# Kernel tuning notes

Hardware: AMD Instinct MI355X
Metric: run time of the kernel (lower is better)

Reference implementation:

```python
import jax, jax.numpy as jnp
import numpy as np

EPS = 1e-5  # BatchNorm eps (torch default)


def setup_inputs() -> dict:
    B, C, H, W = 8, 256, 128, 128
    Cr = C // 4
    key = jax.random.key(0)
    ks = jax.random.split(key, 12)
    s = lambda *sh: 1.0 / np.sqrt(np.prod(sh[1:]) if len(sh) > 1 else sh[0])
    return {
        "x": jax.random.normal(ks[0], (B, C, H, W), jnp.float32),
        "text_feat": jax.random.normal(ks[1], (B, C), jnp.float32),
        # spatial_proj: Conv2d(C,C,1) + BatchNorm2d(C) (eval-mode running stats)
        "proj_w": jax.random.normal(ks[2], (C, C), jnp.float32) * s(C, C),
        "proj_b": jax.random.normal(ks[3], (C,), jnp.float32) * 0.02,
        "bn_gamma": jnp.ones((C,), jnp.float32),
        "bn_beta": jnp.zeros((C,), jnp.float32),
        "bn_mean": jnp.zeros((C,), jnp.float32),
        "bn_var": jnp.ones((C,), jnp.float32),
        # channel_attention: Conv2d(C,C/4,1) -> ReLU -> Conv2d(C/4,C,1) -> Sigmoid
        "ca_w1": jax.random.normal(ks[4], (Cr, C), jnp.float32) * s(Cr, C),
        "ca_b1": jax.random.normal(ks[5], (Cr,), jnp.float32) * 0.02,
        "ca_w2": jax.random.normal(ks[6], (C, Cr), jnp.float32) * s(C, Cr),
        "ca_b2": jax.random.normal(ks[7], (C,), jnp.float32) * 0.02,
        # spatial_attention: Conv2d(2,1,7,padding=3) -> Sigmoid
        "sa_w": jax.random.normal(ks[8], (1, 2, 7, 7), jnp.float32) * s(1, 2 * 49),
        "sa_b": jax.random.normal(ks[9], (1,), jnp.float32) * 0.02,
    }


def _forward(x, text_feat, proj_w, proj_b, bn_gamma, bn_beta, bn_mean, bn_var,
             ca_w1, ca_b1, ca_w2, ca_b2, sa_w, sa_b):
    B, C, H, W = x.shape
    # spatial_proj on the spatially-constant broadcast of text_feat: 1x1 conv + BN
    # + ReLU are pointwise, so compute once per (B,C) vector and broadcast.
    t = jnp.einsum('oc,bc->bo', proj_w, text_feat) + proj_b          # (B,C)
    t = (t - bn_mean) * (bn_gamma / jnp.sqrt(bn_var + EPS)) + bn_beta
    t = jax.nn.relu(t)                                               # (B,C)
    # channel attention: global-avg-pool of a constant map is the value itself
    h = jax.nn.relu(jnp.einsum('rc,bc->br', ca_w1, t) + ca_b1)       # (B,C/4)
    channel_weight = jax.nn.sigmoid(jnp.einsum('cr,br->bc', ca_w2, h) + ca_b2)  # (B,C)
    # spatial attention: channel mean/max are per-batch constants, but the 7x7
    # zero-padded conv has edge effects, so run the real conv on broadcast maps.
    avg_feat = jnp.mean(t, axis=1)                                   # (B,)
    max_feat = jnp.max(t, axis=1)                                    # (B,)
    am = jnp.broadcast_to(jnp.stack([avg_feat, max_feat], axis=1)[:, :, None, None],
                          (B, 2, H, W))                              # (B,2,H,W)
    sw = jax.lax.conv_general_dilated(
        am, sa_w, window_strides=(1, 1), padding=((3, 3), (3, 3)),
        dimension_numbers=('NCHW', 'OIHW', 'NCHW')) + sa_b[None, :, None, None]
    spatial_weight = jax.nn.sigmoid(sw)                              # (B,1,H,W)
    return x * channel_weight[:, :, None, None] * spatial_weight


def reference(x, text_feat, proj_w, proj_b, bn_gamma, bn_beta, bn_mean, bn_var,
              ca_w1, ca_b1, ca_w2, ca_b2, sa_w, sa_b):
    return _forward(x, text_feat, proj_w, proj_b, bn_gamma, bn_beta, bn_mean,
                    bn_var, ca_w1, ca_b1, ca_w2, ca_b2, sa_w, sa_b)
```

## Files before the change

### kernel.cpp

```cpp
#include <hip/hip_runtime.h>
#include <math.h>

#define B 8
#define C 256
#define CR 64
#define H 128
#define W 128
#define HW (H*W)
#define NELEM (B*C*HW)
#define N4 (NELEM/4)
#define PER_BATCH4 (C*HW/4)
#define FUSE_BLOCKS_X 1024
#define FUSE_ITERS 4
#define FUSE_STRIDE (FUSE_BLOCKS_X*256)

typedef float floatx4 __attribute__((ext_vector_type(4)));

__device__ __forceinline__ float sigmoidf_(float z) {
    return 1.0f / (1.0f + expf(-z));
}

__global__ __launch_bounds__(256)
void setup_kernel(const float* __restrict__ tf,
                  const float* __restrict__ pw,
                  const float* __restrict__ pb,
                  const float* __restrict__ g,
                  const float* __restrict__ be,
                  const float* __restrict__ mu,
                  const float* __restrict__ var,
                  const float* __restrict__ w1,
                  const float* __restrict__ b1,
                  const float* __restrict__ w2,
                  const float* __restrict__ b2,
                  const float* __restrict__ saw,
                  const float* __restrict__ sab,
                  float* __restrict__ cw,
                  float* __restrict__ tbl)
{
    const int b   = blockIdx.x;
    const int tid = threadIdx.x;

    __shared__ float tf_sh[C];
    __shared__ float t_sh[C];
    __shared__ float h_sh[CR];
    __shared__ float red[8];
    __shared__ float s_stats[2];
    __shared__ float saw_sh[98];

    tf_sh[tid] = tf[b * C + tid];
    if (tid < 98) saw_sh[tid] = saw[tid];
    __syncthreads();

    float acc = 0.0f;
    {
        const float4* pwr = reinterpret_cast<const float4*>(pw + tid * C);
        #pragma unroll 16
        for (int k4 = 0; k4 < C / 4; ++k4) {
            const float4 wv = pwr[k4];
            const float* tfk = &tf_sh[k4 * 4];
            acc += wv.x * tfk[0] + wv.y * tfk[1] + wv.z * tfk[2] + wv.w * tfk[3];
        }
    }
    float t;
    {
        const float scale = g[tid] * rsqrtf(var[tid] + 1e-5f);
        t = (acc + pb[tid] - mu[tid]) * scale + be[tid];
        t = fmaxf(t, 0.0f);
        t_sh[tid] = t;
    }

    {
        float s = t, m = t;
        #pragma unroll
        for (int off = 32; off > 0; off >>= 1) {
            s += __shfl_down(s, off);
            m  = fmaxf(m, __shfl_down(m, off));
        }
        const int wv_ = tid >> 6;
        if ((tid & 63) == 0) { red[wv_] = s; red[4 + wv_] = m; }
        __syncthreads();
        if (tid == 0) {
            s_stats[0] = (red[0] + red[1] + red[2] + red[3]) * (1.0f / C);
            s_stats[1] = fmaxf(fmaxf(red[4], red[5]), fmaxf(red[6], red[7]));
        }
        __syncthreads();
    }

    if (tid < 49) {
        const int yc = tid / 7, xc = tid % 7;
        const int ky0 = yc < 3 ? 3 - yc : 0;
        const int ky1 = yc > 3 ? 9 - yc : 6;
        const int kx0 = xc < 3 ? 3 - xc : 0;
        const int kx1 = xc > 3 ? 9 - xc : 6;
        float S0 = 0.0f, S1 = 0.0f;
        for (int ky = ky0; ky <= ky1; ++ky)
            for (int kx = kx0; kx <= kx1; ++kx) {
                S0 += saw_sh[ky * 7 + kx];
                S1 += saw_sh[49 + ky * 7 + kx];
            }
        tbl[b * 49 + tid] = sigmoidf_(s_stats[0] * S0 + s_stats[1] * S1 + sab[0]);
    }

    if (tid < CR) {
        float a = b1[tid];
        const float4* w1r = reinterpret_cast<const float4*>(w1 + tid * C);
        #pragma unroll 16
        for (int k4 = 0; k4 < C / 4; ++k4) {
            const float4 wv = w1r[k4];
            const float* tk = &t_sh[k4 * 4];
            a += wv.x * tk[0] + wv.y * tk[1] + wv.z * tk[2] + wv.w * tk[3];
        }
        h_sh[tid] = fmaxf(a, 0.0f);
    }
    __syncthreads();

    {
        float a = b2[tid];
        const float4* w2r = reinterpret_cast<const float4*>(w2 + tid * CR);
        #pragma unroll
        for (int r4 = 0; r4 < CR / 4; ++r4) {
            const float4 wv = w2r[r4];
            const float* hk = &h_sh[r4 * 4];
            a += wv.x * hk[0] + wv.y * hk[1] + wv.z * hk[2] + wv.w * hk[3];
        }
        cw[b * C + tid] = sigmoidf_(a);
    }
}

__global__ __launch_bounds__(256)
void fuse_kernel(const floatx4* __restrict__ x4,
                 const float*   __restrict__ cw,
                 const float*   __restrict__ tbl,
                 floatx4* __restrict__ out4)
{
    __shared__ float cw_sh[C];
    __shared__ float tbl_sh[49];

    const int b   = blockIdx.y;
    const int tid = threadIdx.x;
    cw_sh[tid] = cw[b * C + tid];
    if (tid < 49) tbl_sh[tid] = tbl[b * 49 + tid];
    __syncthreads();

    const int local0 = blockIdx.x * 256 + tid;
    const int s4 = local0 & 4095;
    const int y  = s4 >> 5;
    const int xg = s4 & 31;
    const int yc = y < 3 ? y : (y > 124 ? y - 121 : 3);
    const float* tb = &tbl_sh[yc * 7];
    float s0, s1, s2, s3;
    if (xg == 0)       { s0 = tb[0]; s1 = tb[1]; s2 = tb[2]; s3 = tb[3]; }
    else if (xg == 31) { s0 = tb[3]; s1 = tb[4]; s2 = tb[5]; s3 = tb[6]; }
    else               { s0 = s1 = s2 = s3 = tb[3]; }

    const long base = (long)b * PER_BATCH4 + local0;
    const int  c0   = local0 >> 12;

    floatx4 xs[FUSE_ITERS];
    #pragma unroll
    for (int i = 0; i < FUSE_ITERS; ++i)
        xs[i] = x4[base + (long)i * FUSE_STRIDE];

    #pragma unroll
    for (int i = 0; i < FUSE_ITERS; ++i) {
        const float cwv = cw_sh[c0 + i * (FUSE_STRIDE >> 12)];
        floatx4 o;
        o.x = xs[i].x * cwv * s0;
        o.y = xs[i].y * cwv * s1;
        o.z = xs[i].z * cwv * s2;
        o.w = xs[i].w * cwv * s3;
        __builtin_nontemporal_store(o, &out4[base + (long)i * FUSE_STRIDE]);
    }
}

extern "C" void kernel_launch(void* const* d_in, const int* in_sizes, int n_in,
                              void* d_out, int out_size, void* d_ws, size_t ws_size,
                              hipStream_t stream) {
    const float* x    = (const float*)d_in[0];
    const float* tf   = (const float*)d_in[1];
    const float* pw   = (const float*)d_in[2];
    const float* pb   = (const float*)d_in[3];
    const float* g    = (const float*)d_in[4];
    const float* be   = (const float*)d_in[5];
    const float* mu   = (const float*)d_in[6];
    const float* var  = (const float*)d_in[7];
    const float* w1   = (const float*)d_in[8];
    const float* b1   = (const float*)d_in[9];
    const float* w2   = (const float*)d_in[10];
    const float* b2   = (const float*)d_in[11];
    const float* saw  = (const float*)d_in[12];
    const float* sab  = (const float*)d_in[13];
    float* out = (float*)d_out;

    float* wsf = (float*)d_ws;
    float* cw  = wsf;
    float* tbl = wsf + 2048;

    setup_kernel<<<B, 256, 0, stream>>>(tf, pw, pb, g, be, mu, var,
                                        w1, b1, w2, b2, saw, sab, cw, tbl);
    fuse_kernel<<<dim3(FUSE_BLOCKS_X, B), 256, 0, stream>>>(
        (const floatx4*)x, cw, tbl, (floatx4*)out);
}
```

Before: 67.49 us.

## Split setup into parallel GEMV kernel and attention kernel with split-K reductions

The single 8-block setup kernel becomes two kernels. The first spreads the 256x256 projection GEMV over 64 blocks, with 8 lanes per output channel and a shuffle reduction. The second computes the channel-attention MLP with 4 lanes per hidden unit, prefetching the w1 weights into registers, and unrolls the 7x7 table sum with predication. The aim is to shorten the serial setup latency ahead of the bandwidth-bound fuse kernel, at the cost of one extra kernel launch and a workspace round trip for t.

```diff
diff --git a/kernel.cpp b/kernel.cpp
--- a/kernel.cpp
+++ b/kernel.cpp
@@ -21,56 +21,86 @@
 }
 
 __global__ __launch_bounds__(256)
-void setup_kernel(const float* __restrict__ tf,
-                  const float* __restrict__ pw,
-                  const float* __restrict__ pb,
-                  const float* __restrict__ g,
-                  const float* __restrict__ be,
-                  const float* __restrict__ mu,
-                  const float* __restrict__ var,
-                  const float* __restrict__ w1,
-                  const float* __restrict__ b1,
-                  const float* __restrict__ w2,
-                  const float* __restrict__ b2,
-                  const float* __restrict__ saw,
-                  const float* __restrict__ sab,
-                  float* __restrict__ cw,
-                  float* __restrict__ tbl)
+void gemv_kernel(const float* __restrict__ tf,
+                 const float* __restrict__ pw,
+                 const float* __restrict__ pb,
+                 const float* __restrict__ g,
+                 const float* __restrict__ be,
+                 const float* __restrict__ mu,
+                 const float* __restrict__ var,
+                 float* __restrict__ t_out)
+{
+    const int gx  = blockIdx.x;
+    const int b   = blockIdx.y;
+    const int tid = threadIdx.x;
+
+    __shared__ float tf_sh[C];
+    tf_sh[tid] = tf[b * C + tid];
+
+    const int ch = tid >> 3;
+    const int c  = gx * 32 + ch;
+    const int sl = tid & 7;
+
+    float gc = 0.f, vc = 0.f, pbc = 0.f, muc = 0.f, bec = 0.f;
+    if (sl == 0) { gc = g[c]; vc = var[c]; pbc = pb[c]; muc = mu[c]; bec = be[c]; }
+    __syncthreads();
+
+    float acc = 0.f;
+    {
+        const float4* pwr = reinterpret_cast<const float4*>(pw + c * C + sl * 32);
+        const float*  tfk = &tf_sh[sl * 32];
+        #pragma unroll
+        for (int i = 0; i < 8; ++i) {
+            const float4 wv = pwr[i];
+            acc += wv.x * tfk[4*i] + wv.y * tfk[4*i+1]
+                 + wv.z * tfk[4*i+2] + wv.w * tfk[4*i+3];
+        }
+    }
+    acc += __shfl_xor(acc, 4);
+    acc += __shfl_xor(acc, 2);
+    acc += __shfl_xor(acc, 1);
+    if (sl == 0) {
+        float tv = (acc + pbc - muc) * (gc * rsqrtf(vc + 1e-5f)) + bec;
+        t_out[b * C + c] = fmaxf(tv, 0.f);
+    }
+}
+
+__global__ __launch_bounds__(256)
+void attn_kernel(const float* __restrict__ t_in,
+                 const float* __restrict__ w1,
+                 const float* __restrict__ b1,
+                 const float* __restrict__ w2,
+                 const float* __restrict__ b2,
+                 const float* __restrict__ saw,
+                 const float* __restrict__ sab,
+                 float* __restrict__ cw,
+                 float* __restrict__ tbl)
 {
     const int b   = blockIdx.x;
     const int tid = threadIdx.x;
 
-    __shared__ float tf_sh[C];
     __shared__ float t_sh[C];
     __shared__ float h_sh[CR];
     __shared__ float red[8];
     __shared__ float s_stats[2];
     __shared__ float saw_sh[98];
 
-    tf_sh[tid] = tf[b * C + tid];
+    const float tv = t_in[b * C + tid];
+    t_sh[tid] = tv;
     if (tid < 98) saw_sh[tid] = saw[tid];
-    __syncthreads();
-
-    float acc = 0.0f;
-    {
-        const float4* pwr = reinterpret_cast<const float4*>(pw + tid * C);
-        #pragma unroll 16
-        for (int k4 = 0; k4 < C / 4; ++k4) {
-            const float4 wv = pwr[k4];
-            const float* tfk = &tf_sh[k4 * 4];
-            acc += wv.x * tfk[0] + wv.y * tfk[1] + wv.z * tfk[2] + wv.w * tfk[3];
-        }
-    }
-    float t;
-    {
-        const float scale = g[tid] * rsqrtf(var[tid] + 1e-5f);
-        t = (acc + pb[tid] - mu[tid]) * scale + be[tid];
-        t = fmaxf(t, 0.0f);
-        t_sh[tid] = t;
-    }
-
-    {
-        float s = t, m = t;
+
+    const int r  = tid >> 2;
+    const int sl = tid & 3;
+    float b1r = (sl == 0) ? b1[r] : 0.f;
+    float4 w1v[16];
+    {
+        const float4* w1r = reinterpret_cast<const float4*>(w1 + r * C + sl * 64);
+        #pragma unroll
+        for (int i = 0; i < 16; ++i) w1v[i] = w1r[i];
+    }
+
+    {
+        float s = tv, m = tv;
         #pragma unroll
         for (int off = 32; off > 0; off >>= 1) {
             s += __shfl_down(s, off);
@@ -83,7 +113,32 @@
             s_stats[0] = (red[0] + red[1] + red[2] + red[3]) * (1.0f / C);
             s_stats[1] = fmaxf(fmaxf(red[4], red[5]), fmaxf(red[6], red[7]));
         }
-        __syncthreads();
+    }
+
+    {
+        float hacc = 0.f;
+        const float* tk = &t_sh[sl * 64];
+        #pragma unroll
+        for (int i = 0; i < 16; ++i) {
+            hacc += w1v[i].x * tk[4*i] + w1v[i].y * tk[4*i+1]
+                  + w1v[i].z * tk[4*i+2] + w1v[i].w * tk[4*i+3];
+        }
+        hacc += __shfl_xor(hacc, 2);
+        hacc += __shfl_xor(hacc, 1);
+        if (sl == 0) h_sh[r] = fmaxf(hacc + b1r, 0.f);
+    }
+    __syncthreads();
+
+    {
+        float a = b2[tid];
+        const float4* w2r = reinterpret_cast<const float4*>(w2 + tid * CR);
+        #pragma unroll
+        for (int r4 = 0; r4 < CR / 4; ++r4) {
+            const float4 wv = w2r[r4];
+            const float* hk = &h_sh[r4 * 4];
+            a += wv.x * hk[0] + wv.y * hk[1] + wv.z * hk[2] + wv.w * hk[3];
+        }
+        cw[b * C + tid] = sigmoidf_(a);
     }
 
     if (tid < 49) {
@@ -92,38 +147,16 @@
         const int ky1 = yc > 3 ? 9 - yc : 6;
         const int kx0 = xc < 3 ? 3 - xc : 0;
         const int kx1 = xc > 3 ? 9 - xc : 6;
-        float S0 = 0.0f, S1 = 0.0f;
-        for (int ky = ky0; ky <= ky1; ++ky)
-            for (int kx = kx0; kx <= kx1; ++kx) {
-                S0 += saw_sh[ky * 7 + kx];
-                S1 += saw_sh[49 + ky * 7 + kx];
+        float S0 = 0.f, S1 = 0.f;
+        #pragma unroll
+        for (int ky = 0; ky < 7; ++ky)
+            #pragma unroll
+            for (int kx = 0; kx < 7; ++kx) {
+                const bool in = (ky >= ky0) & (ky <= ky1) & (kx >= kx0) & (kx <= kx1);
+                S0 += in ? saw_sh[ky * 7 + kx]      : 0.f;
+                S1 += in ? saw_sh[49 + ky * 7 + kx] : 0.f;
             }
         tbl[b * 49 + tid] = sigmoidf_(s_stats[0] * S0 + s_stats[1] * S1 + sab[0]);
-    }
-
-    if (tid < CR) {
-        float a = b1[tid];
-        const float4* w1r = reinterpret_cast<const float4*>(w1 + tid * C);
-        #pragma unroll 16
-        for (int k4 = 0; k4 < C / 4; ++k4) {
-            const float4 wv = w1r[k4];
-            const float* tk = &t_sh[k4 * 4];
-            a += wv.x * tk[0] + wv.y * tk[1] + wv.z * tk[2] + wv.w * tk[3];
-        }
-        h_sh[tid] = fmaxf(a, 0.0f);
-    }
-    __syncthreads();
-
-    {
-        float a = b2[tid];
-        const float4* w2r = reinterpret_cast<const float4*>(w2 + tid * CR);
-        #pragma unroll
-        for (int r4 = 0; r4 < CR / 4; ++r4) {
-            const float4 wv = w2r[r4];
-            const float* hk = &h_sh[r4 * 4];
-            a += wv.x * hk[0] + wv.y * hk[1] + wv.z * hk[2] + wv.w * hk[3];
-        }
-        cw[b * C + tid] = sigmoidf_(a);
     }
 }
 
@@ -193,11 +226,12 @@
     float* out = (float*)d_out;
 
     float* wsf = (float*)d_ws;
-    float* cw  = wsf;
-    float* tbl = wsf + 2048;
-
-    setup_kernel<<<B, 256, 0, stream>>>(tf, pw, pb, g, be, mu, var,
-                                        w1, b1, w2, b2, saw, sab, cw, tbl);
+    float* t_  = wsf;
+    float* cw  = wsf + 2048;
+    float* tbl = wsf + 4096;
+
+    gemv_kernel<<<dim3(8, B), 256, 0, stream>>>(tf, pw, pb, g, be, mu, var, t_);
+    attn_kernel<<<B, 256, 0, stream>>>(t_, w1, b1, w2, b2, saw, sab, cw, tbl);
     fuse_kernel<<<dim3(FUSE_BLOCKS_X, B), 256, 0, stream>>>(
         (const floatx4*)x, cw, tbl, (floatx4*)out);
 }
```

After: 56.60 us. 1.19x faster.
